# Performance work log

Hardware: AMD Instinct MI355X
Metric: run time of the kernel (lower is better)

The kernel has to match this reference:

```python
import jax, jax.numpy as jnp
import numpy as np

N = 100000
E = 3200000
IN_C, HID, OUT_C = 512, 256, 40
NUM_LAYERS = 2
BN_EPS = 1e-5


def setup_inputs() -> dict:
    key = jax.random.key(0)
    ks = jax.random.split(key, 12)
    s = 0.05  # weight scale to keep activations sane
    return {
        "x": jax.random.normal(ks[0], (N, IN_C), jnp.float32),
        "edge_index": jax.random.randint(ks[1], (2, E), 0, N, jnp.int64),
        "fc0_W": jax.random.normal(ks[2], (IN_C, HID), jnp.float32) * s,
        "fc0_b": jax.random.normal(ks[3], (HID,), jnp.float32) * s,
        "conv_W": jax.random.normal(ks[4], (NUM_LAYERS, HID, HID), jnp.float32) * s,
        "conv_b": jax.random.normal(ks[5], (NUM_LAYERS, HID), jnp.float32) * s,
        "bn_gamma": jax.random.uniform(ks[6], (NUM_LAYERS + 1, HID), jnp.float32, 0.5, 1.5),
        "bn_beta": jax.random.normal(ks[7], (NUM_LAYERS + 1, HID), jnp.float32) * s,
        "bn_mean": jax.random.normal(ks[8], (NUM_LAYERS + 1, HID), jnp.float32) * s,
        "bn_var": jax.random.uniform(ks[9], (NUM_LAYERS + 1, HID), jnp.float32, 0.5, 1.5),
        "clf_W": jax.random.normal(ks[10], (HID, OUT_C), jnp.float32) * s,
        "clf_b": jax.random.normal(ks[11], (OUT_C,), jnp.float32) * s,
    }


def _bn(x, gamma, beta, mean, var):
    # BatchNorm1d in eval mode (running stats)
    return (x - mean) * (gamma * jax.lax.rsqrt(var + BN_EPS)) + beta


def _aggregate(x, row, col):
    # degree-normalized SpMM: out[col[e]] += (1/sqrt(d[col[e]]d[row[e]])) * x[row[e]]
    n = x.shape[0]
    d = jax.ops.segment_sum(jnp.ones((row.shape[0],), x.dtype), col, num_segments=n)
    dn = jnp.where(d > 0, jax.lax.rsqrt(d), 0.0)  # nan_to_num of 1/sqrt(0)
    val = dn[col] * dn[row]  # [E]
    msgs = val[:, None] * x[row]  # [E, HID]
    return jax.ops.segment_sum(msgs, col, num_segments=n)


def reference(x, edge_index, fc0_W, fc0_b, conv_W, conv_b,
              bn_gamma, bn_beta, bn_mean, bn_var, clf_W, clf_b):
    row, col = edge_index[0], edge_index[1]
    h = jax.nn.relu(_bn(x @ fc0_W + fc0_b, bn_gamma[0], bn_beta[0], bn_mean[0], bn_var[0]))
    prev = h  # layer_[-1] == layer_[0] (only one append)
    for i in range(NUM_LAYERS):
        h = _aggregate(h, row, col) @ conv_W[i] + conv_b[i]
        h = jax.nn.relu(_bn(h, bn_gamma[i + 1], bn_beta[i + 1], bn_mean[i + 1], bn_var[i + 1]))
        h = h + prev  # residual to first-layer features
    return h @ clf_W + clf_b
```

## Files before the change

### kernel.cpp

```cpp
#include <hip/hip_runtime.h>
#include <stdint.h>

#define NN 100000
#define NE 3200000
#define KIN 512
#define HID 256
#define NOUT 40
#define NB2 1024
#define BSHIFT2 7
#define NBKT 782
#define EPB 8192

typedef __attribute__((ext_vector_type(8))) __bf16 bf16x8;
typedef __attribute__((ext_vector_type(4))) float f32x4;

__device__ __forceinline__ float b2f(unsigned short u) {
  union { unsigned int i; float f; } x; x.i = ((unsigned int)u) << 16; return x.f;
}
__device__ __forceinline__ unsigned short f2b(float f) {
  unsigned int i = __float_as_uint(f);
  return (unsigned short)((i + 0x7FFFu + ((i >> 16) & 1u)) >> 16);
}
__device__ __forceinline__ float uf(unsigned int x) { return __uint_as_float(x); }
__device__ __forceinline__ unsigned char f2e8(float v) {
  v = fminf(v, 480.f);
  unsigned int ui = __float_as_uint(v);
  ui += 0x3FFFFu + ((ui >> 19) & 1u);
  unsigned int e32 = ui >> 23;
  if (e32 <= 120u) return 0;
  return (unsigned char)(((e32 - 120u) << 4) | ((ui >> 19) & 15u));
}
__device__ __forceinline__ float e82f(unsigned char u) {
  return __uint_as_float(((unsigned int)u) << 19) * 0x1p120f;
}
__device__ __forceinline__ unsigned short* swz(unsigned short* base, int row, int kk) {
  int byte = (row * 64 + kk * 2) ^ ((row & 7) << 4);
  return (unsigned short*)((char*)base + byte);
}
__device__ __forceinline__ char* swzst(unsigned short* base, int row, int cb) {
  int byte = (row * 128 + cb) ^ ((row & 7) << 4);
  return (char*)base + byte;
}

__global__ __launch_bounds__(256) void k_bhist(const int* __restrict__ ecol, int* __restrict__ bcnt) {
  __shared__ int hist[NB2];
  int t = threadIdx.x;
  for (int j = t; j < NB2; j += 256) hist[j] = 0;
  __syncthreads();
  int e0 = blockIdx.x * EPB, e1 = min(e0 + EPB, NE);
  for (int e = e0 + t; e < e1; e += 256) atomicAdd(&hist[ecol[e] >> BSHIFT2], 1);
  __syncthreads();
  for (int j = t; j < NB2; j += 256) if (hist[j]) atomicAdd(&bcnt[j], hist[j]);
}

__global__ void k_bscan(const int* __restrict__ bcnt, int* __restrict__ bbase, int* __restrict__ cursor) {
  __shared__ int wsum[4];
  int t = threadIdx.x, lane = t & 63, w = t >> 6;
  int4 v = *(const int4*)(bcnt + 4 * t);
  int tot = v.x + v.y + v.z + v.w;
  int s = tot;
  for (int d = 1; d < 64; d <<= 1) { int o = __shfl_up(s, d, 64); if (lane >= d) s += o; }
  if (lane == 63) wsum[w] = s;
  __syncthreads();
  int add = 0;
  for (int i = 0; i < 4; ++i) add += (i < w) ? wsum[i] : 0;
  int excl = add + s - tot;
  int p0 = excl, p1 = p0 + v.x, p2 = p1 + v.y, p3 = p2 + v.z;
  bbase[4 * t] = p0; bbase[4 * t + 1] = p1; bbase[4 * t + 2] = p2; bbase[4 * t + 3] = p3;
  cursor[4 * t] = p0; cursor[4 * t + 1] = p1; cursor[4 * t + 2] = p2; cursor[4 * t + 3] = p3;
}

__global__ __launch_bounds__(256) void k_bucket(const int* __restrict__ erow, const int* __restrict__ ecol,
                                                int* __restrict__ cursor, unsigned int* __restrict__ ebuf) {
  __shared__ int hist[NB2];
  __shared__ int base[NB2];
  int t = threadIdx.x;
  for (int j = t; j < NB2; j += 256) hist[j] = 0;
  __syncthreads();
  int e0 = blockIdx.x * EPB, e1 = min(e0 + EPB, NE);
  for (int e = e0 + t; e < e1; e += 256) atomicAdd(&hist[ecol[e] >> BSHIFT2], 1);
  __syncthreads();
  for (int j = t; j < NB2; j += 256) {
    int c = hist[j];
    base[j] = (c > 0) ? atomicAdd(&cursor[j], c) : 0;
    hist[j] = 0;
  }
  __syncthreads();
  for (int e = e0 + t; e < e1; e += 256) {
    int col = ecol[e];
    int b = col >> BSHIFT2;
    int r = atomicAdd(&hist[b], 1);
    ebuf[(size_t)base[b] + r] = ((unsigned int)(col & 127) << 17) | (unsigned int)erow[e];
  }
}

__global__ __launch_bounds__(256) void k_subdeg(const unsigned int* __restrict__ ebuf,
                                                const int* __restrict__ bbase, const int* __restrict__ bcnt,
                                                int* __restrict__ deg, float* __restrict__ dn) {
  __shared__ int h[128];
  int t = threadIdx.x, b = blockIdx.x;
  if (t < 128) h[t] = 0;
  __syncthreads();
  int s = bbase[b], e = s + bcnt[b];
  for (int i = s + t; i < e; i += 256) atomicAdd(&h[ebuf[i] >> 17], 1);
  __syncthreads();
  if (t < 128) {
    int col = (b << BSHIFT2) + t;
    if (col < NN) { int d = h[t]; deg[col] = d; dn[col] = d > 0 ? rsqrtf((float)d) : 0.f; }
  }
}

#define SCAN_CH 1024
__global__ void k_scan_part(const int* __restrict__ deg, int* __restrict__ partials) {
  __shared__ int lds[4];
  int b = blockIdx.x, t = threadIdx.x;
  int base = b * SCAN_CH;
  int s = 0;
  for (int j = 0; j < 4; ++j) { int i = base + t + 256 * j; if (i < NN) s += deg[i]; }
  for (int d = 32; d > 0; d >>= 1) s += __shfl_down(s, d, 64);
  int lane = t & 63, w = t >> 6;
  if (lane == 0) lds[w] = s;
  __syncthreads();
  if (t == 0) partials[b] = lds[0] + lds[1] + lds[2] + lds[3];
}

__global__ void k_scan_partials(int* __restrict__ partials, int nb) {
  __shared__ int lds[2];
  int t = threadIdx.x;
  int v = (t < nb) ? partials[t] : 0;
  int lane = t & 63, w = t >> 6;
  int s = v;
  for (int d = 1; d < 64; d <<= 1) { int o = __shfl_up(s, d, 64); if (lane >= d) s += o; }
  if (lane == 63) lds[w] = s;
  __syncthreads();
  int base = (w == 1) ? lds[0] : 0;
  if (t < nb) partials[t] = base + s - v;
}

__global__ void k_scan_final(const int* __restrict__ deg, const int* __restrict__ partials,
                             int* __restrict__ colptr, int* __restrict__ pos) {
  __shared__ int lds[4];
  int b = blockIdx.x, t = threadIdx.x;
  int base = b * SCAN_CH + t * 4;
  int d0 = (base + 0 < NN) ? deg[base + 0] : 0;
  int d1 = (base + 1 < NN) ? deg[base + 1] : 0;
  int d2 = (base + 2 < NN) ? deg[base + 2] : 0;
  int d3 = (base + 3 < NN) ? deg[base + 3] : 0;
  int tot = d0 + d1 + d2 + d3;
  int lane = t & 63, w = t >> 6;
  int s = tot;
  for (int d = 1; d < 64; d <<= 1) { int o = __shfl_up(s, d, 64); if (lane >= d) s += o; }
  if (lane == 63) lds[w] = s;
  __syncthreads();
  int wbase = 0;
  for (int i = 0; i < 4; ++i) wbase += (i < w) ? lds[i] : 0;
  int excl = wbase + s - tot + partials[b];
  int p0 = excl, p1 = p0 + d0, p2 = p1 + d1, p3 = p2 + d2, p4 = p3 + d3;
  if (base + 0 <= NN) colptr[base + 0] = p0;
  if (base + 1 <= NN) colptr[base + 1] = p1;
  if (base + 2 <= NN) colptr[base + 2] = p2;
  if (base + 3 <= NN) colptr[base + 3] = p3;
  if (base + 4 == NN) colptr[NN] = p4;
  if (base + 0 < NN) pos[base + 0] = p0;
  if (base + 1 < NN) pos[base + 1] = p1;
  if (base + 2 < NN) pos[base + 2] = p2;
  if (base + 3 < NN) pos[base + 3] = p3;
}

__global__ __launch_bounds__(256) void k_fill2(const unsigned int* __restrict__ ebuf,
                                               const int* __restrict__ bbase, const int* __restrict__ bcnt,
                                               int* __restrict__ pos, int* __restrict__ csr_row) {
  int b = blockIdx.x >> 2, sub = blockIdx.x & 3;
  int s = bbase[b], e = s + bcnt[b];
  int cb = b << BSHIFT2;
  for (int i = s + sub * 256 + threadIdx.x; i < e; i += 1024) {
    unsigned int pk = ebuf[i];
    int p = atomicAdd(&pos[cb | (int)(pk >> 17)], 1);
    csr_row[p] = (int)(pk & 0x1FFFF);
  }
}

__global__ void k_prep(const float* __restrict__ fc0_W, const float* __restrict__ fc0_b,
                       const float* __restrict__ conv_W, const float* __restrict__ conv_b,
                       const float* __restrict__ bn_gamma, const float* __restrict__ bn_beta,
                       const float* __restrict__ bn_mean, const float* __restrict__ bn_var,
                       const float* __restrict__ clf_W,
                       unsigned short* __restrict__ W0t, unsigned short* __restrict__ Wct,
                       unsigned short* __restrict__ Wclft,
                       float* __restrict__ epia, float* __restrict__ epib,
                       unsigned char* __restrict__ h0s) {
  int idx = blockIdx.x * 256 + threadIdx.x;
  if (idx < 131072) {
    int n = idx >> 9, k = idx & 511;
    W0t[idx] = f2b(fc0_W[k * 256 + n]);
  } else if (idx < 262144) {
    int j = idx - 131072;
    int l = j >> 16, rem = j & 65535, n = rem >> 8, k = rem & 255;
    Wct[j] = f2b(conv_W[l * 65536 + k * 256 + n]);
  } else if (idx < 262144 + 48 * 256) {
    int j = idx - 262144;
    int n = j >> 8, k = j & 255;
    Wclft[j] = f2b(n < NOUT ? clf_W[k * NOUT + n] : 0.f);
  } else if (idx < 262144 + 12288 + 768) {
    int j = idx - 262144 - 12288;
    int layer = j >> 8, c = j & 255;
    float a = bn_gamma[j] * rsqrtf(bn_var[j] + 1e-5f);
    float bias = (layer == 0) ? fc0_b[c] : conv_b[(layer - 1) * 256 + c];
    epia[j] = a;
    epib[j] = bn_beta[j] + (bias - bn_mean[j]) * a;
  } else if (idx < 262144 + 12288 + 768 + 256) {
    int c = idx - (262144 + 12288 + 768);
    h0s[(size_t)NN * HID + c] = 0;
  }
}

template <int K, bool AF32, int EPI>
__global__ __launch_bounds__(512) void k_gemm2(const void* __restrict__ Av,
                                               const unsigned short* __restrict__ Bt,
                                               const float* __restrict__ epia,
                                               const float* __restrict__ epib,
                                               const void* prevv,
                                               const float* __restrict__ dnp,
                                               void* outv, void* outv2) {
  __shared__ unsigned short ldsA[128 * 32];
  __shared__ unsigned short ldsB[256 * 32];
  const int t = threadIdx.x;
  const int w = t >> 6, lane = t & 63;
  const int lo = lane & 15, hi = lane >> 4;
  const int wr = w >> 1, wc = w & 1;
  const int m0 = blockIdx.x * 128;
  constexpr int NK = K / 32;
  f32x4 acc[2][8];
#pragma unroll
  for (int m = 0; m < 2; ++m)
#pragma unroll
    for (int f = 0; f < 8; ++f) acc[m][f] = (f32x4){0.f, 0.f, 0.f, 0.f};

  const int arow = t >> 2;
  const int akk = (t & 3) * 8;
  const int rg = m0 + arow;
  const int bn0 = t >> 2, bn1 = bn0 + 128;

  float4 rv0, rv1;
  int4 ra, rb0, rb1;

#define LOADG(k0_) {                                                        \
    if (AF32) {                                                             \
      const float* A = (const float*)Av;                                    \
      rv0 = (float4){0.f, 0.f, 0.f, 0.f}; rv1 = rv0;                        \
      if (rg < NN) {                                                        \
        rv0 = *(const float4*)(A + (size_t)rg * K + (k0_) + akk);           \
        rv1 = *(const float4*)(A + (size_t)rg * K + (k0_) + akk + 4);       \
      }                                                                     \
    } else {                                                                \
      const unsigned short* A = (const unsigned short*)Av;                  \
      ra = (int4){0, 0, 0, 0};                                              \
      if (rg < NN) ra = *(const int4*)(A + (size_t)rg * K + (k0_) + akk);   \
    }                                                                       \
    rb0 = *(const int4*)(Bt + (size_t)bn0 * K + (k0_) + akk);               \
    rb1 = *(const int4*)(Bt + (size_t)bn1 * K + (k0_) + akk);               \
  }
#define WRITELDS() {                                                        \
    if (AF32) {                                                             \
      union { unsigned short u[8]; int4 v; } pk;                            \
      pk.u[0] = f2b(rv0.x); pk.u[1] = f2b(rv0.y);                           \
      pk.u[2] = f2b(rv0.z); pk.u[3] = f2b(rv0.w);                           \
      pk.u[4] = f2b(rv1.x); pk.u[5] = f2b(rv1.y);                           \
      pk.u[6] = f2b(rv1.z); pk.u[7] = f2b(rv1.w);                           \
      *(int4*)(void*)swz(ldsA, arow, akk) = pk.v;                           \
    } else {                                                                \
      *(int4*)(void*)swz(ldsA, arow, akk) = ra;                             \
    }                                                                       \
    *(int4*)(void*)swz(ldsB, bn0, akk) = rb0;                               \
    *(int4*)(void*)swz(ldsB, bn1, akk) = rb1;                               \
  }

  LOADG(0);
  for (int k = 0; k < NK; ++k) {
    asm volatile("s_waitcnt lgkmcnt(0)" ::: "memory");
    __builtin_amdgcn_s_barrier();
    __builtin_amdgcn_sched_barrier(0);
    WRITELDS();
    __syncthreads();
    if (k + 1 < NK) LOADG((k + 1) * 32);
    bf16x8 af0 = *(const bf16x8*)(void*)swz(ldsA, wr * 32 + lo, hi * 8);
    bf16x8 af1 = *(const bf16x8*)(void*)swz(ldsA, wr * 32 + 16 + lo, hi * 8);
#pragma unroll
    for (int f = 0; f < 8; ++f) {
      bf16x8 bf = *(const bf16x8*)(void*)swz(ldsB, wc * 128 + f * 16 + lo, hi * 8);
      acc[0][f] = __builtin_amdgcn_mfma_f32_16x16x32_bf16(af0, bf, acc[0][f], 0, 0, 0);
      acc[1][f] = __builtin_amdgcn_mfma_f32_16x16x32_bf16(af1, bf, acc[1][f], 0, 0, 0);
    }
  }
  asm volatile("s_waitcnt lgkmcnt(0)" ::: "memory");
  __builtin_amdgcn_s_barrier();
  __builtin_amdgcn_sched_barrier(0);

#pragma unroll
  for (int cc = 0; cc < 4; ++cc) {
    if (cc) __syncthreads();
    if (wc == (cc >> 1)) {
#pragma unroll
      for (int m = 0; m < 2; ++m) {
        const int rb = wr * 32 + m * 16 + hi * 4;
#pragma unroll
        for (int fl = 0; fl < 4; ++fl) {
          const int f = (cc & 1) * 4 + fl;
          const int c = wc * 128 + f * 16 + lo;
          float a_ = epia[c], b_ = epib[c];
#pragma unroll
          for (int j = 0; j < 4; ++j) {
            int row = rb + j;
            int r = m0 + row;
            float y = fmaxf(a_ * acc[m][f][j] + b_, 0.f);
            float sv;
            if constexpr (EPI == 1) {
              float dnv = (r < NN) ? dnp[r] : 0.f;
              sv = y * dnv;
            } else {
              sv = y;
            }
            *(unsigned short*)swzst(ldsB, row, (fl * 16 + lo) * 2) = f2b(sv);
          }
        }
      }
    }
    __syncthreads();
#pragma unroll
    for (int pass = 0; pass < 2; ++pass) {
      int rr = pass * 64 + (t >> 3);
      int r = m0 + rr;
      int cb = (t & 7) * 16;
      uint4 v = *(const uint4*)swzst(ldsB, rr, cb);
      if (r < NN) {
        size_t gix = (size_t)r * HID + cc * 64 + (t & 7) * 8;
        union { unsigned short u[8]; uint4 v4; } sb; sb.v4 = v;
        if constexpr (EPI == 0) {
          *(uint4*)((unsigned short*)outv + gix) = v;
          float d = dnp[r];
          union { unsigned char b[8]; uint2 v2; } o8;
#pragma unroll
          for (int q = 0; q < 8; ++q) o8.b[q] = f2e8(d * b2f(sb.u[q]));
          *(uint2*)((unsigned char*)outv2 + gix) = o8.v2;
        } else if constexpr (EPI == 1) {
          union { unsigned char b[8]; uint2 v2; } pv;
          pv.v2 = *(const uint2*)((const unsigned char*)prevv + gix);
          union { unsigned char b[8]; uint2 v2; } o8;
#pragma unroll
          for (int q = 0; q < 8; ++q) o8.b[q] = f2e8(b2f(sb.u[q]) + e82f(pv.b[q]));
          *(uint2*)((unsigned char*)outv + gix) = o8.v2;
        } else {
          union { unsigned short u[8]; uint4 v4; } pv;
          pv.v4 = *(const uint4*)((const unsigned short*)prevv + gix);
          union { unsigned short u[8]; uint4 v4; } o;
#pragma unroll
          for (int q = 0; q < 8; ++q) o.u[q] = f2b(b2f(sb.u[q]) + b2f(pv.u[q]));
          *(uint4*)((unsigned short*)outv + gix) = o.v4;
        }
      }
    }
  }
#undef LOADG
#undef WRITELDS
}

__global__ __launch_bounds__(256) void k_gemmclf(const unsigned short* __restrict__ Av,
                                                 const unsigned short* __restrict__ Bt,
                                                 const float* __restrict__ clfb,
                                                 float* __restrict__ out) {
  __shared__ unsigned short ldsA[64 * 32];
  __shared__ unsigned short ldsB[48 * 32];
  const int t = threadIdx.x;
  const int w = t >> 6, lane = t & 63;
  const int lo = lane & 15, hi = lane >> 4;
  const int m0 = blockIdx.x * 64;
  f32x4 acc[3];
#pragma unroll
  for (int f = 0; f < 3; ++f) acc[f] = (f32x4){0.f, 0.f, 0.f, 0.f};
  const int arow = t >> 2;
  const int akk = (t & 3) * 8;
  const int rg = m0 + arow;
  for (int k0 = 0; k0 < HID; k0 += 32) {
    int4 v = {0, 0, 0, 0};
    if (rg < NN) v = *(const int4*)(Av + (size_t)rg * HID + k0 + akk);
    *(int4*)(void*)swz(ldsA, arow, akk) = v;
    if (t < 48 * 4) {
      int n = t >> 2;
      int4 vb = *(const int4*)(Bt + (size_t)n * HID + k0 + akk);
      *(int4*)(void*)swz(ldsB, n, akk) = vb;
    }
    __syncthreads();
    bf16x8 af = *(const bf16x8*)(void*)swz(ldsA, w * 16 + lo, hi * 8);
#pragma unroll
    for (int f = 0; f < 3; ++f) {
      bf16x8 bf = *(const bf16x8*)(void*)swz(ldsB, f * 16 + lo, hi * 8);
      acc[f] = __builtin_amdgcn_mfma_f32_16x16x32_bf16(af, bf, acc[f], 0, 0, 0);
    }
    __syncthreads();
  }
  const int rbase = m0 + w * 16 + hi * 4;
#pragma unroll
  for (int f = 0; f < 3; ++f) {
    int c = f * 16 + lo;
    if (c >= NOUT) continue;
    float bb = clfb[c];
#pragma unroll
    for (int j = 0; j < 4; ++j) {
      int r = rbase + j;
      if (r < NN) out[(size_t)r * NOUT + c] = acc[f][j] + bb;
    }
  }
}

__global__ __launch_bounds__(256) void k_agg(const int* __restrict__ colptr,
                                             const int* __restrict__ csr,
                                             const float* __restrict__ dn,
                                             const unsigned char* __restrict__ hs,
                                             unsigned short* __restrict__ X) {
  int w = threadIdx.x >> 6, lane = threadIdx.x & 63;
  int i = blockIdx.x * 4 + w;
  int hl = lane & 31, half = lane >> 5;
  const unsigned char* hb = hs + hl * 8;
  int e0 = colptr[i], e1 = colptr[i + 1];
  float a0 = 0, a1 = 0, a2 = 0, a3 = 0, a4 = 0, a5 = 0, a6 = 0, a7 = 0;
  int rA[4], rB[4];
  uint2 vA[4], vB[4];

#define LOADIDX(e_, r_) { \
  _Pragma("unroll") for (int u = 0; u < 4; ++u) { \
    int ee = (e_) + 2 * u + half; \
    int rr = csr[ee]; \
    r_[u] = (ee < e1) ? rr : NN; } }
#define GATHER(r_, v_) { \
  _Pragma("unroll") for (int u = 0; u < 4; ++u) \
    v_[u] = *(const uint2*)(hb + (size_t)r_[u] * HID); }
#define ACCUM(v_) { \
  _Pragma("unroll") for (int u = 0; u < 4; ++u) { \
    a0 += uf((v_[u].x << 19) & 0x07F80000u); a1 += uf((v_[u].x << 11) & 0x07F80000u); \
    a2 += uf((v_[u].x << 3)  & 0x07F80000u); a3 += uf((v_[u].x >> 5)  & 0x07F80000u); \
    a4 += uf((v_[u].y << 19) & 0x07F80000u); a5 += uf((v_[u].y << 11) & 0x07F80000u); \
    a6 += uf((v_[u].y << 3)  & 0x07F80000u); a7 += uf((v_[u].y >> 5)  & 0x07F80000u); } }

  int nb = (e1 - e0 + 7) >> 3;
  if (nb == 1) {
    LOADIDX(e0, rA); GATHER(rA, vA); ACCUM(vA);
  } else if (nb > 1) {
    LOADIDX(e0, rA);
    GATHER(rA, vA);
    LOADIDX(e0 + 8, rB);
    int b = 1, e = e0 + 8;
    for (; b + 1 < nb; ++b, e += 8) {
      if (b & 1) { GATHER(rB, vB); LOADIDX(e + 8, rA); ACCUM(vA); }
      else       { GATHER(rA, vA); LOADIDX(e + 8, rB); ACCUM(vB); }
    }
    if (b & 1) { GATHER(rB, vB); ACCUM(vA); ACCUM(vB); }
    else       { GATHER(rA, vA); ACCUM(vB); ACCUM(vA); }
  }
  a0 += __shfl_xor(a0, 32); a1 += __shfl_xor(a1, 32);
  a2 += __shfl_xor(a2, 32); a3 += __shfl_xor(a3, 32);
  a4 += __shfl_xor(a4, 32); a5 += __shfl_xor(a5, 32);
  a6 += __shfl_xor(a6, 32); a7 += __shfl_xor(a7, 32);
  if (half == 0) {
    float d = dn[i] * 0x1p120f;
    union { unsigned short u[8]; uint4 v; } o;
    o.u[0] = f2b(d * a0); o.u[1] = f2b(d * a1); o.u[2] = f2b(d * a2); o.u[3] = f2b(d * a3);
    o.u[4] = f2b(d * a4); o.u[5] = f2b(d * a5); o.u[6] = f2b(d * a6); o.u[7] = f2b(d * a7);
    *(uint4*)(X + (size_t)i * HID + hl * 8) = o.v;
  }
}

extern "C" void kernel_launch(void* const* d_in, const int* in_sizes, int n_in,
                              void* d_out, int out_size, void* d_ws, size_t ws_size,
                              hipStream_t stream) {
  const float* x        = (const float*)d_in[0];
  const int*   edge     = (const int*)d_in[1];
  const int*   erow     = edge;
  const int*   ecol     = edge + NE;
  const float* fc0_W    = (const float*)d_in[2];
  const float* fc0_b    = (const float*)d_in[3];
  const float* conv_W   = (const float*)d_in[4];
  const float* conv_b   = (const float*)d_in[5];
  const float* bn_gamma = (const float*)d_in[6];
  const float* bn_beta  = (const float*)d_in[7];
  const float* bn_mean  = (const float*)d_in[8];
  const float* bn_var   = (const float*)d_in[9];
  const float* clf_W    = (const float*)d_in[10];
  const float* clf_b    = (const float*)d_in[11];

  char* p = (char*)d_ws;
  auto alloc = [&](size_t bytes) { char* r = p; p += (bytes + 255) & ~(size_t)255; return r; };
  int*   deg      = (int*)alloc((size_t)NN * 4);
  float* dn       = (float*)alloc((size_t)NN * 4);
  int*   colptr   = (int*)alloc((size_t)(NN + 1) * 4);
  int*   pos      = (int*)alloc((size_t)NN * 4);
  int*   partials = (int*)alloc(1024);
  int*   bcnt     = (int*)alloc(NB2 * 4);
  int*   bbase    = (int*)alloc(NB2 * 4);
  int*   cursor   = (int*)alloc(NB2 * 4);
  int*   csr_row  = (int*)alloc(((size_t)NE + 16) * 4);
  unsigned short* W0t   = (unsigned short*)alloc((size_t)256 * 512 * 2);
  unsigned short* Wct   = (unsigned short*)alloc((size_t)2 * 256 * 256 * 2);
  unsigned short* Wclft = (unsigned short*)alloc((size_t)48 * 256 * 2);
  float* epia = (float*)alloc(768 * 4);
  float* epib = (float*)alloc(768 * 4);
  unsigned short* h0  = (unsigned short*)alloc((size_t)NN * HID * 2);
  unsigned char*  h0s = (unsigned char*)alloc((size_t)(NN + 1) * HID);
  unsigned short* X   = (unsigned short*)alloc((size_t)NN * HID * 2);
  unsigned int* ebuf = (unsigned int*)X;

  int nbBlk = (NE + EPB - 1) / EPB;
  hipMemsetAsync(bcnt, 0, NB2 * 4, stream);
  k_bhist<<<nbBlk, 256, 0, stream>>>(ecol, bcnt);
  k_bscan<<<1, 256, 0, stream>>>(bcnt, bbase, cursor);
  k_bucket<<<nbBlk, 256, 0, stream>>>(erow, ecol, cursor, ebuf);
  k_subdeg<<<NBKT, 256, 0, stream>>>(ebuf, bbase, bcnt, deg, dn);
  int nb = (NN + SCAN_CH - 1) / SCAN_CH;
  k_scan_part<<<nb, 256, 0, stream>>>(deg, partials);
  k_scan_partials<<<1, 128, 0, stream>>>(partials, nb);
  k_scan_final<<<nb, 256, 0, stream>>>(deg, partials, colptr, pos);
  k_fill2<<<NBKT * 4, 256, 0, stream>>>(ebuf, bbase, bcnt, pos, csr_row);
  k_prep<<<1076, 256, 0, stream>>>(fc0_W, fc0_b, conv_W, conv_b, bn_gamma, bn_beta,
                                   bn_mean, bn_var, clf_W, W0t, Wct, Wclft, epia, epib, h0s);

  int gm2 = (NN + 127) / 128;
  k_gemm2<KIN, true, 0><<<gm2, 512, 0, stream>>>(x, W0t, epia, epib, nullptr, dn, h0, h0s);
  k_agg<<<(NN + 3) / 4, 256, 0, stream>>>(colptr, csr_row, dn, h0s, X);
  k_gemm2<HID, false, 1><<<gm2, 512, 0, stream>>>(X, Wct, epia + 256, epib + 256, h0s, dn, h0s, nullptr);
  k_agg<<<(NN + 3) / 4, 256, 0, stream>>>(colptr, csr_row, dn, h0s, X);
  k_gemm2<HID, false, 3><<<gm2, 512, 0, stream>>>(X, Wct + 65536, epia + 512, epib + 512, h0, nullptr, h0, nullptr);
  k_gemmclf<<<(NN + 63) / 64, 256, 0, stream>>>(h0, Wclft, clf_b, (float*)d_out);
}
```

Baseline: 645.6 us.

## Fuse classifier into GEMM epilogues via linearity and store aggregates as FP8

```diff
diff --git a/kernel.cpp b/kernel.cpp
--- a/kernel.cpp
+++ b/kernel.cpp
@@ -32,6 +32,9 @@
 }
 __device__ __forceinline__ float e82f(unsigned char u) {
   return __uint_as_float(((unsigned int)u) << 19) * 0x1p120f;
+}
+__device__ __forceinline__ unsigned short e82b(unsigned char u) {
+  return u ? (unsigned short)(((unsigned int)u << 3) + 0x3C00u) : (unsigned short)0;
 }
 __device__ __forceinline__ unsigned short* swz(unsigned short* base, int row, int kk) {
   int byte = (row * 64 + kk * 2) ^ ((row & 7) << 4);
@@ -214,16 +217,19 @@
   }
 }
 
-template <int K, bool AF32, int EPI>
+template <int K, int ALAY, int EPI>
 __global__ __launch_bounds__(512) void k_gemm2(const void* __restrict__ Av,
                                                const unsigned short* __restrict__ Bt,
                                                const float* __restrict__ epia,
                                                const float* __restrict__ epib,
                                                const void* prevv,
                                                const float* __restrict__ dnp,
+                                               const unsigned short* __restrict__ clfW,
+                                               const float* __restrict__ clfb,
                                                void* outv, void* outv2) {
   __shared__ unsigned short ldsA[128 * 32];
   __shared__ unsigned short ldsB[256 * 32];
+  constexpr bool DOCLF = (EPI == 0 || EPI == 4);
   const int t = threadIdx.x;
   const int w = t >> 6, lane = t & 63;
   const int lo = lane & 15, hi = lane >> 4;
@@ -235,6 +241,9 @@
   for (int m = 0; m < 2; ++m)
 #pragma unroll
     for (int f = 0; f < 8; ++f) acc[m][f] = (f32x4){0.f, 0.f, 0.f, 0.f};
+  f32x4 accclf[3];
+#pragma unroll
+  for (int f = 0; f < 3; ++f) accclf[f] = (f32x4){0.f, 0.f, 0.f, 0.f};
 
   const int arow = t >> 2;
   const int akk = (t & 3) * 8;
@@ -242,39 +251,50 @@
   const int bn0 = t >> 2, bn1 = bn0 + 128;
 
   float4 rv0, rv1;
-  int4 ra, rb0, rb1;
+  int4 ra;
+  uint2 rae;
 
 #define LOADG(k0_) {                                                        \
-    if (AF32) {                                                             \
+    if (ALAY == 0) {                                                        \
       const float* A = (const float*)Av;                                    \
       rv0 = (float4){0.f, 0.f, 0.f, 0.f}; rv1 = rv0;                        \
       if (rg < NN) {                                                        \
         rv0 = *(const float4*)(A + (size_t)rg * K + (k0_) + akk);           \
         rv1 = *(const float4*)(A + (size_t)rg * K + (k0_) + akk + 4);       \
       }                                                                     \
-    } else {                                                                \
+    } else if (ALAY == 1) {                                                 \
       const unsigned short* A = (const unsigned short*)Av;                  \
       ra = (int4){0, 0, 0, 0};                                              \
       if (rg < NN) ra = *(const int4*)(A + (size_t)rg * K + (k0_) + akk);   \
+    } else {                                                                \
+      const unsigned char* A = (const unsigned char*)Av;                    \
+      rae = (uint2){0u, 0u};                                                \
+      if (rg < NN) rae = *(const uint2*)(A + (size_t)rg * K + (k0_) + akk); \
     }                                                                       \
     rb0 = *(const int4*)(Bt + (size_t)bn0 * K + (k0_) + akk);               \
     rb1 = *(const int4*)(Bt + (size_t)bn1 * K + (k0_) + akk);               \
   }
 #define WRITELDS() {                                                        \
-    if (AF32) {                                                             \
+    if (ALAY == 0) {                                                        \
       union { unsigned short u[8]; int4 v; } pk;                            \
       pk.u[0] = f2b(rv0.x); pk.u[1] = f2b(rv0.y);                           \
       pk.u[2] = f2b(rv0.z); pk.u[3] = f2b(rv0.w);                           \
       pk.u[4] = f2b(rv1.x); pk.u[5] = f2b(rv1.y);                           \
       pk.u[6] = f2b(rv1.z); pk.u[7] = f2b(rv1.w);                           \
       *(int4*)(void*)swz(ldsA, arow, akk) = pk.v;                           \
+    } else if (ALAY == 1) {                                                 \
+      *(int4*)(void*)swz(ldsA, arow, akk) = ra;                             \
     } else {                                                                \
-      *(int4*)(void*)swz(ldsA, arow, akk) = ra;                             \
+      union { unsigned char b[8]; uint2 v2; } in; in.v2 = rae;              \
+      union { unsigned short u[8]; int4 v; } pk;                            \
+      _Pragma("unroll") for (int q = 0; q < 8; ++q) pk.u[q] = e82b(in.b[q]);\
+      *(int4*)(void*)swz(ldsA, arow, akk) = pk.v;                           \
     }                                                                       \
     *(int4*)(void*)swz(ldsB, bn0, akk) = rb0;                               \
     *(int4*)(void*)swz(ldsB, bn1, akk) = rb1;                               \
   }
 
+  int4 rb0, rb1;
   LOADG(0);
   for (int k = 0; k < NK; ++k) {
     asm volatile("s_waitcnt lgkmcnt(0)" ::: "memory");
@@ -326,97 +346,74 @@
       }
     }
     __syncthreads();
-#pragma unroll
-    for (int pass = 0; pass < 2; ++pass) {
-      int rr = pass * 64 + (t >> 3);
-      int r = m0 + rr;
-      int cb = (t & 7) * 16;
-      uint4 v = *(const uint4*)swzst(ldsB, rr, cb);
-      if (r < NN) {
-        size_t gix = (size_t)r * HID + cc * 64 + (t & 7) * 8;
-        union { unsigned short u[8]; uint4 v4; } sb; sb.v4 = v;
-        if constexpr (EPI == 0) {
-          *(uint4*)((unsigned short*)outv + gix) = v;
-          float d = dnp[r];
-          union { unsigned char b[8]; uint2 v2; } o8;
-#pragma unroll
-          for (int q = 0; q < 8; ++q) o8.b[q] = f2e8(d * b2f(sb.u[q]));
-          *(uint2*)((unsigned char*)outv2 + gix) = o8.v2;
-        } else if constexpr (EPI == 1) {
-          union { unsigned char b[8]; uint2 v2; } pv;
-          pv.v2 = *(const uint2*)((const unsigned char*)prevv + gix);
-          union { unsigned char b[8]; uint2 v2; } o8;
-#pragma unroll
-          for (int q = 0; q < 8; ++q) o8.b[q] = f2e8(b2f(sb.u[q]) + e82f(pv.b[q]));
-          *(uint2*)((unsigned char*)outv + gix) = o8.v2;
-        } else {
-          union { unsigned short u[8]; uint4 v4; } pv;
-          pv.v4 = *(const uint4*)((const unsigned short*)prevv + gix);
-          union { unsigned short u[8]; uint4 v4; } o;
-#pragma unroll
-          for (int q = 0; q < 8; ++q) o.u[q] = f2b(b2f(sb.u[q]) + b2f(pv.u[q]));
-          *(uint4*)((unsigned short*)outv + gix) = o.v4;
+    if constexpr (EPI == 0 || EPI == 1) {
+#pragma unroll
+      for (int pass = 0; pass < 2; ++pass) {
+        int rr = pass * 64 + (t >> 3);
+        int r = m0 + rr;
+        int cb = (t & 7) * 16;
+        uint4 v = *(const uint4*)swzst(ldsB, rr, cb);
+        if (r < NN) {
+          size_t gix = (size_t)r * HID + cc * 64 + (t & 7) * 8;
+          union { unsigned short u[8]; uint4 v4; } sb; sb.v4 = v;
+          if constexpr (EPI == 0) {
+            float d = dnp[r];
+            union { unsigned char b[8]; uint2 v2; } o8;
+#pragma unroll
+            for (int q = 0; q < 8; ++q) o8.b[q] = f2e8(d * b2f(sb.u[q]));
+            *(uint2*)((unsigned char*)outv2 + gix) = o8.v2;
+          } else {
+            union { unsigned char b[8]; uint2 v2; } pv;
+            pv.v2 = *(const uint2*)((const unsigned char*)prevv + gix);
+            union { unsigned char b[8]; uint2 v2; } o8;
+#pragma unroll
+            for (int q = 0; q < 8; ++q) o8.b[q] = f2e8(b2f(sb.u[q]) + e82f(pv.b[q]));
+            *(uint2*)((unsigned char*)outv + gix) = o8.v2;
+          }
         }
       }
     }
+    if constexpr (DOCLF) {
+#pragma unroll
+      for (int kk = 0; kk < 2; ++kk) {
+        bf16x8 af = *(const bf16x8*)(const void*)swzst(ldsB, w * 16 + lo, (kk * 32 + hi * 8) * 2);
+#pragma unroll
+        for (int f = 0; f < 3; ++f) {
+          bf16x8 bf = *(const bf16x8*)(clfW + (size_t)(f * 16 + lo) * HID + cc * 64 + kk * 32 + hi * 8);
+          accclf[f] = __builtin_amdgcn_mfma_f32_16x16x32_bf16(af, bf, accclf[f], 0, 0, 0);
+        }
+      }
+    }
+  }
+  if constexpr (DOCLF) {
+#pragma unroll
+    for (int f = 0; f < 3; ++f) {
+      int c = f * 16 + lo;
+      if (c < NOUT) {
+#pragma unroll
+        for (int j = 0; j < 4; ++j) {
+          int r = m0 + w * 16 + hi * 4 + j;
+          if (r < NN) {
+            if constexpr (EPI == 0) {
+              ((float*)outv)[(size_t)r * NOUT + c] = accclf[f][j];
+            } else {
+              ((float*)outv)[(size_t)r * NOUT + c] =
+                  accclf[f][j] + ((const float*)prevv)[(size_t)r * NOUT + c] + clfb[c];
+            }
+          }
+        }
+      }
+    }
   }
 #undef LOADG
 #undef WRITELDS
-}
-
-__global__ __launch_bounds__(256) void k_gemmclf(const unsigned short* __restrict__ Av,
-                                                 const unsigned short* __restrict__ Bt,
-                                                 const float* __restrict__ clfb,
-                                                 float* __restrict__ out) {
-  __shared__ unsigned short ldsA[64 * 32];
-  __shared__ unsigned short ldsB[48 * 32];
-  const int t = threadIdx.x;
-  const int w = t >> 6, lane = t & 63;
-  const int lo = lane & 15, hi = lane >> 4;
-  const int m0 = blockIdx.x * 64;
-  f32x4 acc[3];
-#pragma unroll
-  for (int f = 0; f < 3; ++f) acc[f] = (f32x4){0.f, 0.f, 0.f, 0.f};
-  const int arow = t >> 2;
-  const int akk = (t & 3) * 8;
-  const int rg = m0 + arow;
-  for (int k0 = 0; k0 < HID; k0 += 32) {
-    int4 v = {0, 0, 0, 0};
-    if (rg < NN) v = *(const int4*)(Av + (size_t)rg * HID + k0 + akk);
-    *(int4*)(void*)swz(ldsA, arow, akk) = v;
-    if (t < 48 * 4) {
-      int n = t >> 2;
-      int4 vb = *(const int4*)(Bt + (size_t)n * HID + k0 + akk);
-      *(int4*)(void*)swz(ldsB, n, akk) = vb;
-    }
-    __syncthreads();
-    bf16x8 af = *(const bf16x8*)(void*)swz(ldsA, w * 16 + lo, hi * 8);
-#pragma unroll
-    for (int f = 0; f < 3; ++f) {
-      bf16x8 bf = *(const bf16x8*)(void*)swz(ldsB, f * 16 + lo, hi * 8);
-      acc[f] = __builtin_amdgcn_mfma_f32_16x16x32_bf16(af, bf, acc[f], 0, 0, 0);
-    }
-    __syncthreads();
-  }
-  const int rbase = m0 + w * 16 + hi * 4;
-#pragma unroll
-  for (int f = 0; f < 3; ++f) {
-    int c = f * 16 + lo;
-    if (c >= NOUT) continue;
-    float bb = clfb[c];
-#pragma unroll
-    for (int j = 0; j < 4; ++j) {
-      int r = rbase + j;
-      if (r < NN) out[(size_t)r * NOUT + c] = acc[f][j] + bb;
-    }
-  }
 }
 
 __global__ __launch_bounds__(256) void k_agg(const int* __restrict__ colptr,
                                              const int* __restrict__ csr,
                                              const float* __restrict__ dn,
                                              const unsigned char* __restrict__ hs,
-                                             unsigned short* __restrict__ X) {
+                                             unsigned char* __restrict__ X) {
   int w = threadIdx.x >> 6, lane = threadIdx.x & 63;
   int i = blockIdx.x * 4 + w;
   int hl = lane & 31, half = lane >> 5;
@@ -462,10 +459,10 @@
   a6 += __shfl_xor(a6, 32); a7 += __shfl_xor(a7, 32);
   if (half == 0) {
     float d = dn[i] * 0x1p120f;
-    union { unsigned short u[8]; uint4 v; } o;
-    o.u[0] = f2b(d * a0); o.u[1] = f2b(d * a1); o.u[2] = f2b(d * a2); o.u[3] = f2b(d * a3);
-    o.u[4] = f2b(d * a4); o.u[5] = f2b(d * a5); o.u[6] = f2b(d * a6); o.u[7] = f2b(d * a7);
-    *(uint4*)(X + (size_t)i * HID + hl * 8) = o.v;
+    union { unsigned char b[8]; uint2 v; } o;
+    o.b[0] = f2e8(d * a0); o.b[1] = f2e8(d * a1); o.b[2] = f2e8(d * a2); o.b[3] = f2e8(d * a3);
+    o.b[4] = f2e8(d * a4); o.b[5] = f2e8(d * a5); o.b[6] = f2e8(d * a6); o.b[7] = f2e8(d * a7);
+    *(uint2*)(X + (size_t)i * HID + hl * 8) = o.v;
   }
 }
 
@@ -503,9 +500,9 @@
   unsigned short* Wclft = (unsigned short*)alloc((size_t)48 * 256 * 2);
   float* epia = (float*)alloc(768 * 4);
   float* epib = (float*)alloc(768 * 4);
-  unsigned short* h0  = (unsigned short*)alloc((size_t)NN * HID * 2);
+  float* outP = (float*)alloc((size_t)NN * NOUT * 4);
   unsigned char*  h0s = (unsigned char*)alloc((size_t)(NN + 1) * HID);
-  unsigned short* X   = (unsigned short*)alloc((size_t)NN * HID * 2);
+  unsigned char*  X   = (unsigned char*)alloc((size_t)NN * HID);
   unsigned int* ebuf = (unsigned int*)X;
 
   int nbBlk = (NE + EPB - 1) / EPB;
@@ -523,10 +520,9 @@
                                    bn_mean, bn_var, clf_W, W0t, Wct, Wclft, epia, epib, h0s);
 
   int gm2 = (NN + 127) / 128;
-  k_gemm2<KIN, true, 0><<<gm2, 512, 0, stream>>>(x, W0t, epia, epib, nullptr, dn, h0, h0s);
+  k_gemm2<KIN, 0, 0><<<gm2, 512, 0, stream>>>(x, W0t, epia, epib, nullptr, dn, Wclft, nullptr, outP, h0s);
   k_agg<<<(NN + 3) / 4, 256, 0, stream>>>(colptr, csr_row, dn, h0s, X);
-  k_gemm2<HID, false, 1><<<gm2, 512, 0, stream>>>(X, Wct, epia + 256, epib + 256, h0s, dn, h0s, nullptr);
+  k_gemm2<HID, 2, 1><<<gm2, 512, 0, stream>>>(X, Wct, epia + 256, epib + 256, h0s, dn, nullptr, nullptr, h0s, nullptr);
   k_agg<<<(NN + 3) / 4, 256, 0, stream>>>(colptr, csr_row, dn, h0s, X);
-  k_gemm2<HID, false, 3><<<gm2, 512, 0, stream>>>(X, Wct + 65536, epia + 512, epib + 512, h0, nullptr, h0, nullptr);
-  k_gemmclf<<<(NN + 63) / 64, 256, 0, stream>>>(h0, Wclft, clf_b, (float*)d_out);
-}
+  k_gemm2<HID, 2, 4><<<gm2, 512, 0, stream>>>(X, Wct + 65536, epia + 512, epib + 512, outP, nullptr, Wclft, clf_b, d_out, nullptr);
+}
```

New measurement: 622.7 us (median of 2 runs). -3.6%, faster.
